# Kernel tuning notes

Measured on AMD Instinct MI355X. Metric: run time of the kernel, lower is better.

Reference implementation:

```python
import jax, jax.numpy as jnp
import numpy as np

D_MODEL = 1024
N_HEADS = 16
D_K = D_MODEL // N_HEADS


def setup_inputs() -> dict:
    key = jax.random.key(0)
    k1, k2, k3, k4, k5 = jax.random.split(key, 5)
    B, S = 2, 2048
    scale = 1.0 / np.sqrt(D_MODEL)
    return {
        "query": jax.random.normal(k1, (B, S, D_MODEL), dtype=jnp.float32),
        "mask": jnp.ones((B, S, S), dtype=jnp.int32),
        "W_qkv": jax.random.normal(k2, (D_MODEL, 3 * D_MODEL), dtype=jnp.float32) * scale,
        "b_qkv": jax.random.normal(k3, (3 * D_MODEL,), dtype=jnp.float32) * 0.02,
        "W_out": jax.random.normal(k4, (D_MODEL, D_MODEL), dtype=jnp.float32) * scale,
        "b_out": jax.random.normal(k5, (D_MODEL,), dtype=jnp.float32) * 0.02,
    }


def reference(query, mask, W_qkv, b_qkv, W_out, b_out):
    B, S, _ = query.shape
    # fused QKV projection (all from query, matching the torch module)
    qkv = query @ W_qkv + b_qkv                      # [B, S, 3*D]
    q, k, v = jnp.split(qkv, 3, axis=-1)
    # [B, H, S, d_k]
    q = q.reshape(B, S, N_HEADS, D_K).transpose(0, 2, 1, 3)
    k = k.reshape(B, S, N_HEADS, D_K).transpose(0, 2, 1, 3)
    v = v.reshape(B, S, N_HEADS, D_K).transpose(0, 2, 1, 3)
    # scaled dot-product attention with explicit scores
    scores = jnp.einsum("bhqd,bhkd->bhqk", q, k) / jnp.sqrt(jnp.float32(D_K))
    m = mask[:, None, :, :]                           # [B, 1, S, S] broadcast over heads
    scores = jnp.where(m == 0, jnp.float32(-1e9), scores)
    attn = jax.nn.softmax(scores, axis=-1)           # dropout p=0 in eval -> identity
    ctx = jnp.einsum("bhqk,bhkd->bhqd", attn, v)     # [B, H, S, d_k]
    ctx = ctx.transpose(0, 2, 1, 3).reshape(B, S, D_MODEL)
    return ctx @ W_out + b_out
```

## Files before the change

### kernel.cpp

```cpp
#include <hip/hip_runtime.h>
#include <stdint.h>
#include <stddef.h>

#define S_LEN 2048
#define NB    2
#define DM    1024
#define NH    16
#define DKH   64
#define NTOK  4096
#define QKV_N 3072
#define QSCALE 0.18033688f

typedef __attribute__((ext_vector_type(4))) float floatx4;
using half2v = __attribute__((ext_vector_type(2))) _Float16;
using half4v = __attribute__((ext_vector_type(4))) _Float16;
using half8v = __attribute__((ext_vector_type(8))) _Float16;
using fp16x2 = __attribute__((ext_vector_type(2))) __fp16;

#if __has_builtin(__builtin_amdgcn_exp2f)
#define EXP2F __builtin_amdgcn_exp2f
#else
#define EXP2F exp2f
#endif

__device__ __forceinline__ void glds16(const void* g, void* l) {
    __builtin_amdgcn_global_load_lds((const __attribute__((address_space(1))) void*)g,
                                     (__attribute__((address_space(3))) void*)l,
                                     16, 0, 0);
}

__global__ __launch_bounds__(256) void cast_f16_kernel(const float* __restrict__ in,
                                                       _Float16* __restrict__ out, int n4) {
    int i = blockIdx.x * blockDim.x + threadIdx.x;
    if (i < n4) {
        float4 v = ((const float4*)in)[i];
        half4v o = {(_Float16)v.x, (_Float16)v.y, (_Float16)v.z, (_Float16)v.w};
        ((half4v*)out)[i] = o;
    }
}

__global__ __launch_bounds__(1024) void transpose_cast_kernel(const float* __restrict__ in,
                                                              _Float16* __restrict__ out,
                                                              int R, int C) {
    __shared__ float t[32][33];
    int c0 = blockIdx.x * 32, r0 = blockIdx.y * 32;
    int x = threadIdx.x, y = threadIdx.y;
    t[y][x] = in[(size_t)(r0 + y) * C + c0 + x];
    __syncthreads();
    out[(size_t)(c0 + y) * R + r0 + x] = (_Float16)t[x][y];
}

__global__ __launch_bounds__(256) void mask_reduce_kernel(const int* __restrict__ mask,
                                                          int* __restrict__ f, int n4) {
    int i = blockIdx.x * blockDim.x + threadIdx.x;
    if (i < n4) {
        int4 v = ((const int4*)mask)[i];
        if (v.x == 0 || v.y == 0 || v.z == 0 || v.w == 0) *f = 0;
    }
}

__global__ __launch_bounds__(256) void transpose_v_kernel(const _Float16* __restrict__ qkv,
                                                          _Float16* __restrict__ vt) {
    __shared__ _Float16 t[64][68];
    int st = blockIdx.x * 64, h = blockIdx.y, b = blockIdx.z;
    int tid = threadIdx.x;
    #pragma unroll
    for (int p = 0; p < 4; ++p) {
        int idx = p * 1024 + tid * 4;
        int sl = idx >> 6, d0 = idx & 63;
        half4v v = *(const half4v*)(qkv + (size_t)(b * S_LEN + st + sl) * QKV_N + 2 * DM + h * DKH + d0);
        t[d0 + 0][sl] = v.x; t[d0 + 1][sl] = v.y; t[d0 + 2][sl] = v.z; t[d0 + 3][sl] = v.w;
    }
    __syncthreads();
    #pragma unroll
    for (int p = 0; p < 4; ++p) {
        int idx = p * 1024 + tid * 4;
        int d = idx >> 6, s0 = idx & 63;
        half4v v = {t[d][s0], t[d][s0 + 1], t[d][s0 + 2], t[d][s0 + 3]};
        *(half4v*)(vt + ((size_t)(b * NH + h) * DKH + d) * S_LEN + st + s0) = v;
    }
}

template <int FINAL, int BN>
__global__ __launch_bounds__(256) void gemm_bt_kernel(const _Float16* __restrict__ A,
                                                      const _Float16* __restrict__ Bt,
                                                      const float* __restrict__ bias,
                                                      float* __restrict__ Cf,
                                                      _Float16* __restrict__ Ch,
                                                      int M, int N, int K) {
    constexpr int NJ = BN / 32;
    __shared__ _Float16 As[128 * 64];
    __shared__ _Float16 Bs[BN * 64];

    const int nt = blockIdx.x, mt = blockIdx.y;
    const int tid = threadIdx.x, wave = tid >> 6, lane = tid & 63;
    const int quad = lane >> 4, l16 = lane & 15;
    const int wm = wave >> 1, wn = wave & 1;

    floatx4 acc[4][NJ];
    #pragma unroll
    for (int i = 0; i < 4; ++i)
        #pragma unroll
        for (int j = 0; j < NJ; ++j)
            #pragma unroll
            for (int r = 0; r < 4; ++r) acc[i][j][r] = 0.0f;

    const _Float16* Ab = A + (size_t)mt * 128 * K;
    const _Float16* Bb = Bt + (size_t)nt * BN * K;

    for (int kt = 0; kt < K; kt += 64) {
        #pragma unroll
        for (int p = 0; p < 4; ++p) {
            int slot = p * 256 + wave * 64 + lane;
            int row = slot >> 3, cc = slot & 7, c = cc ^ (row & 7);
            glds16(Ab + (size_t)row * K + kt + c * 8, As + (size_t)(p * 256 + wave * 64) * 8);
        }
        #pragma unroll
        for (int p = 0; p < BN / 32; ++p) {
            int slot = p * 256 + wave * 64 + lane;
            int row = slot >> 3, cc = slot & 7, c = cc ^ (row & 7);
            glds16(Bb + (size_t)row * K + kt + c * 8, Bs + (size_t)(p * 256 + wave * 64) * 8);
        }
        __syncthreads();

        #pragma unroll
        for (int kk = 0; kk < 2; ++kk) {
            half8v af[4], bfr[NJ];
            #pragma unroll
            for (int i = 0; i < 4; ++i) {
                int row = wm * 64 + i * 16 + l16;
                int c = (kk * 4 + quad) ^ (row & 7);
                af[i] = *(const half8v*)(As + row * 64 + c * 8);
            }
            #pragma unroll
            for (int j = 0; j < NJ; ++j) {
                int row = wn * (BN / 2) + j * 16 + l16;
                int c = (kk * 4 + quad) ^ (row & 7);
                bfr[j] = *(const half8v*)(Bs + row * 64 + c * 8);
            }
            #pragma unroll
            for (int i = 0; i < 4; ++i)
                #pragma unroll
                for (int j = 0; j < NJ; ++j)
                    acc[i][j] = __builtin_amdgcn_mfma_f32_16x16x32_f16(af[i], bfr[j], acc[i][j], 0, 0, 0);
        }
        __syncthreads();
    }

    #pragma unroll
    for (int j = 0; j < NJ; ++j) {
        int n = nt * BN + wn * (BN / 2) + j * 16 + l16;
        float bv = bias[n];
        float sc = (!FINAL && n < DM) ? QSCALE : 1.0f;
        #pragma unroll
        for (int i = 0; i < 4; ++i) {
            int m0 = mt * 128 + wm * 64 + i * 16 + quad * 4;
            #pragma unroll
            for (int r = 0; r < 4; ++r) {
                float v = (acc[i][j][r] + bv) * sc;
                if (FINAL) Cf[(size_t)(m0 + r) * N + n] = v;
                else       Ch[(size_t)(m0 + r) * QKV_N + n] = (_Float16)v;
            }
        }
    }
}

__global__ __launch_bounds__(256) void flash_kernel(const _Float16* __restrict__ qkv,
                                                    const _Float16* __restrict__ vt,
                                                    const int* __restrict__ mask,
                                                    const int* __restrict__ flag,
                                                    _Float16* __restrict__ Opart,
                                                    float* __restrict__ Lpart) {
    __shared__ _Float16 Ks[128 * 64];
    __shared__ _Float16 Vs[64 * 128];

    const int bh = blockIdx.x, qt = blockIdx.y, ks = blockIdx.z;
    const int b = bh >> 4, h = bh & 15;
    const int tid = threadIdx.x, wave = tid >> 6, lane = tid & 63;
    const int quad = lane >> 4, l16 = lane & 15;
    const int allones = (*flag != 0);

    const _Float16* qrow0 = qkv + (size_t)(b * S_LEN + qt * 128 + wave * 32 + l16) * QKV_N + h * DKH;
    const _Float16* qrow1 = qrow0 + (size_t)16 * QKV_N;
    half8v qa0 = *(const half8v*)(qrow0 + quad * 8);
    half8v qa1 = *(const half8v*)(qrow0 + 32 + quad * 8);
    half8v qb0 = *(const half8v*)(qrow1 + quad * 8);
    half8v qb1 = *(const half8v*)(qrow1 + 32 + quad * 8);

    const _Float16* kbase = qkv + (size_t)b * S_LEN * QKV_N + DM + h * DKH;
    const _Float16* vbase = vt + (size_t)(b * NH + h) * DKH * S_LEN;

    floatx4 oa[4], ob[4];
    #pragma unroll
    for (int c = 0; c < 4; ++c)
        #pragma unroll
        for (int r = 0; r < 4; ++r) { oa[c][r] = 0.0f; ob[c][r] = 0.0f; }
    float lsa = 0.0f, lsb = 0.0f;

    for (int kt = ks * 8; kt < ks * 8 + 8; ++kt) {
        #pragma unroll
        for (int p = 0; p < 4; ++p) {
            int slot = p * 256 + wave * 64 + lane;
            int row = slot >> 3, cc = slot & 7, c = cc ^ (row & 7);
            glds16(kbase + (size_t)(kt * 128 + row) * QKV_N + c * 8,
                   Ks + (size_t)(p * 256 + wave * 64) * 8);
        }
        #pragma unroll
        for (int p = 0; p < 4; ++p) {
            int slot = p * 256 + wave * 64 + lane;
            int row = slot >> 4, cc = slot & 15, c = cc ^ (row & 15);
            glds16(vbase + (size_t)row * S_LEN + kt * 128 + c * 8,
                   Vs + (size_t)(p * 256 + wave * 64) * 8);
        }
        __syncthreads();

        half4v pa[8], pb[8];
        #pragma unroll
        for (int j = 0; j < 8; ++j) {
            int rowk = j * 16 + l16;
            half8v a0 = *(const half8v*)(Ks + rowk * 64 + ((quad) ^ (rowk & 7)) * 8);
            half8v a1 = *(const half8v*)(Ks + rowk * 64 + ((4 + quad) ^ (rowk & 7)) * 8);
            floatx4 za, zb;
            #pragma unroll
            for (int r = 0; r < 4; ++r) { za[r] = 0.0f; zb[r] = 0.0f; }
            za = __builtin_amdgcn_mfma_f32_16x16x32_f16(a0, qa0, za, 0, 0, 0);
            za = __builtin_amdgcn_mfma_f32_16x16x32_f16(a1, qa1, za, 0, 0, 0);
            zb = __builtin_amdgcn_mfma_f32_16x16x32_f16(a0, qb0, zb, 0, 0, 0);
            zb = __builtin_amdgcn_mfma_f32_16x16x32_f16(a1, qb1, zb, 0, 0, 0);

            if (!allones) {
                for (int r = 0; r < 4; ++r) {
                    int s = kt * 128 + j * 16 + quad * 4 + r;
                    int qA = qt * 128 + wave * 32 + l16;
                    if (mask[((size_t)b * S_LEN + qA) * S_LEN + s] == 0) za[r] = -1e9f;
                    if (mask[((size_t)b * S_LEN + qA + 16) * S_LEN + s] == 0) zb[r] = -1e9f;
                }
            }

            float p0 = EXP2F(za[0]), p1 = EXP2F(za[1]), p2 = EXP2F(za[2]), p3 = EXP2F(za[3]);
            lsa += (p0 + p1) + (p2 + p3);
            fp16x2 lo = __builtin_amdgcn_cvt_pkrtz(p0, p1);
            fp16x2 hi = __builtin_amdgcn_cvt_pkrtz(p2, p3);
            half2v lo2 = __builtin_bit_cast(half2v, lo);
            half2v hi2 = __builtin_bit_cast(half2v, hi);
            half4v pka = {lo2.x, lo2.y, hi2.x, hi2.y};
            pa[j] = pka;

            p0 = EXP2F(zb[0]); p1 = EXP2F(zb[1]); p2 = EXP2F(zb[2]); p3 = EXP2F(zb[3]);
            lsb += (p0 + p1) + (p2 + p3);
            lo = __builtin_amdgcn_cvt_pkrtz(p0, p1);
            hi = __builtin_amdgcn_cvt_pkrtz(p2, p3);
            lo2 = __builtin_bit_cast(half2v, lo);
            hi2 = __builtin_bit_cast(half2v, hi);
            half4v pkb = {lo2.x, lo2.y, hi2.x, hi2.y};
            pb[j] = pkb;
        }

        #pragma unroll
        for (int j = 0; j < 8; ++j) {
            int g = 2 * j + (quad >> 1);
            #pragma unroll
            for (int c = 0; c < 4; ++c) {
                int rowv = c * 16 + l16;
                half4v bv = *(const half4v*)(Vs + rowv * 128 + ((g ^ (rowv & 15)) * 8) + (quad & 1) * 4);
                oa[c] = __builtin_amdgcn_mfma_f32_16x16x16f16(pa[j], bv, oa[c], 0, 0, 0);
                ob[c] = __builtin_amdgcn_mfma_f32_16x16x16f16(pb[j], bv, ob[c], 0, 0, 0);
            }
        }
        __syncthreads();
    }

    lsa += __shfl_xor(lsa, 16); lsa += __shfl_xor(lsa, 32);
    lsb += __shfl_xor(lsb, 16); lsb += __shfl_xor(lsb, 32);
    float lia[4], lib[4];
    #pragma unroll
    for (int r = 0; r < 4; ++r) {
        int src = (lane & 48) | ((lane >> 4) * 4 + r);
        float la_ = __shfl(lsa, src), lb_ = __shfl(lsb, src);
        lia[r] = la_ > 0.0f ? 1.0f / la_ : 0.0f;
        lib[r] = lb_ > 0.0f ? 1.0f / lb_ : 0.0f;
    }

    const size_t obase = ((size_t)(ks * 32 + bh) * 16 + qt) * (128 * 64);
    #pragma unroll
    for (int c = 0; c < 4; ++c)
        #pragma unroll
        for (int r = 0; r < 4; ++r) {
            int qq = wave * 32 + quad * 4 + r;
            Opart[obase + (size_t)qq * 64 + c * 16 + l16]        = (_Float16)(oa[c][r] * lia[r]);
            Opart[obase + (size_t)(qq + 16) * 64 + c * 16 + l16] = (_Float16)(ob[c][r] * lib[r]);
        }
    const int lbase = ((ks * 32 + bh) * 16 + qt) * 128;
    if (quad == 0) Lpart[lbase + wave * 32 + l16] = lsa;
    if (quad == 1) Lpart[lbase + wave * 32 + 16 + l16] = lsb;
}

__global__ __launch_bounds__(256) void combine_kernel(const _Float16* __restrict__ Opart,
                                                      const float* __restrict__ Lpart,
                                                      _Float16* __restrict__ ctx) {
    const int bh = blockIdx.x, qt = blockIdx.y;
    const int b = bh >> 4, h = bh & 15;
    const _Float16* Oa = Opart + ((size_t)(0 * 32 + bh) * 16 + qt) * (128 * 64);
    const _Float16* Ob = Opart + ((size_t)(1 * 32 + bh) * 16 + qt) * (128 * 64);
    const float* La = Lpart + ((0 * 32 + bh) * 16 + qt) * 128;
    const float* Lb = Lpart + ((1 * 32 + bh) * 16 + qt) * 128;
    #pragma unroll
    for (int k = 0; k < 4; ++k) {
        int i8 = k * 256 + threadIdx.x;
        int q = i8 >> 3, d0 = (i8 & 7) * 8;
        float la = La[q], lb = Lb[q];
        float s = la + lb;
        float w = s > 0.0f ? 1.0f / s : 0.0f;
        float wa = la * w, wb = lb * w;
        half8v va = *(const half8v*)(Oa + (size_t)i8 * 8);
        half8v vb = *(const half8v*)(Ob + (size_t)i8 * 8);
        half8v o;
        #pragma unroll
        for (int e = 0; e < 8; ++e)
            o[e] = (_Float16)((float)va[e] * wa + (float)vb[e] * wb);
        *(half8v*)(ctx + (size_t)(b * S_LEN + qt * 128 + q) * DM + h * DKH + d0) = o;
    }
}

extern "C" void kernel_launch(void* const* d_in, const int* in_sizes, int n_in,
                              void* d_out, int out_size, void* d_ws, size_t ws_size,
                              hipStream_t stream) {
    const float* query = (const float*)d_in[0];
    const int*   mask  = (const int*)d_in[1];
    const float* W_qkv = (const float*)d_in[2];
    const float* b_qkv = (const float*)d_in[3];
    const float* W_out = (const float*)d_in[4];
    const float* b_out = (const float*)d_in[5];
    float* out = (float*)d_out;

    char* w = (char*)d_ws;
    _Float16* qh    = (_Float16*)w;  w += (size_t)NTOK * DM * 2;
    _Float16* wqt   = (_Float16*)w;  w += (size_t)QKV_N * DM * 2;
    _Float16* wot   = (_Float16*)w;  w += (size_t)DM * DM * 2;
    _Float16* qkvh  = (_Float16*)w;  w += (size_t)NTOK * QKV_N * 2;
    _Float16* vt    = (_Float16*)w;  w += (size_t)NB * NH * DKH * S_LEN * 2;
    _Float16* Opart = (_Float16*)w;  w += (size_t)2 * NB * NH * 16 * 128 * 64 * 2;
    float*    Lpart = (float*)w;     w += (size_t)2 * NB * NH * 16 * 128 * 4;
    int*      flag  = (int*)w;
    _Float16* ctxh = qh;

    cast_f16_kernel<<<(NTOK * DM / 4 + 255) / 256, 256, 0, stream>>>(query, qh, NTOK * DM / 4);
    transpose_cast_kernel<<<dim3(QKV_N / 32, DM / 32), dim3(32, 32), 0, stream>>>(W_qkv, wqt, DM, QKV_N);
    transpose_cast_kernel<<<dim3(DM / 32, DM / 32), dim3(32, 32), 0, stream>>>(W_out, wot, DM, DM);
    hipMemsetAsync(flag, 1, 4, stream);
    mask_reduce_kernel<<<(NB * S_LEN * S_LEN / 4 + 255) / 256, 256, 0, stream>>>(
        mask, flag, NB * S_LEN * S_LEN / 4);

    gemm_bt_kernel<0, 128><<<dim3(QKV_N / 128, NTOK / 128), 256, 0, stream>>>(
        qh, wqt, b_qkv, nullptr, qkvh, NTOK, QKV_N, DM);

    transpose_v_kernel<<<dim3(S_LEN / 64, NH, NB), 256, 0, stream>>>(qkvh, vt);

    flash_kernel<<<dim3(NB * NH, S_LEN / 128, 2), 256, 0, stream>>>(
        qkvh, vt, mask, flag, Opart, Lpart);

    combine_kernel<<<dim3(NB * NH, S_LEN / 128), 256, 0, stream>>>(Opart, Lpart, ctxh);

    gemm_bt_kernel<1, 64><<<dim3(DM / 64, NTOK / 128), 256, 0, stream>>>(
        ctxh, wot, b_out, out, nullptr, NTOK, DM, DM);
}
```

Before: 231.9 us.

## Drop split-K attention and combine kernel, use 256-key tiles in flash

```diff
diff --git a/kernel.cpp b/kernel.cpp
--- a/kernel.cpp
+++ b/kernel.cpp
@@ -169,12 +169,11 @@
                                                     const _Float16* __restrict__ vt,
                                                     const int* __restrict__ mask,
                                                     const int* __restrict__ flag,
-                                                    _Float16* __restrict__ Opart,
-                                                    float* __restrict__ Lpart) {
-    __shared__ _Float16 Ks[128 * 64];
-    __shared__ _Float16 Vs[64 * 128];
-
-    const int bh = blockIdx.x, qt = blockIdx.y, ks = blockIdx.z;
+                                                    _Float16* __restrict__ ctx) {
+    __shared__ _Float16 Ks[256 * 64];
+    __shared__ _Float16 Vs[64 * 256];
+
+    const int bh = blockIdx.x, qt = blockIdx.y;
     const int b = bh >> 4, h = bh & 15;
     const int tid = threadIdx.x, wave = tid >> 6, lane = tid & 63;
     const int quad = lane >> 4, l16 = lane & 15;
@@ -197,74 +196,77 @@
         for (int r = 0; r < 4; ++r) { oa[c][r] = 0.0f; ob[c][r] = 0.0f; }
     float lsa = 0.0f, lsb = 0.0f;
 
-    for (int kt = ks * 8; kt < ks * 8 + 8; ++kt) {
-        #pragma unroll
-        for (int p = 0; p < 4; ++p) {
+    for (int kt = 0; kt < S_LEN / 256; ++kt) {
+        #pragma unroll
+        for (int p = 0; p < 8; ++p) {
             int slot = p * 256 + wave * 64 + lane;
             int row = slot >> 3, cc = slot & 7, c = cc ^ (row & 7);
-            glds16(kbase + (size_t)(kt * 128 + row) * QKV_N + c * 8,
+            glds16(kbase + (size_t)(kt * 256 + row) * QKV_N + c * 8,
                    Ks + (size_t)(p * 256 + wave * 64) * 8);
         }
         #pragma unroll
-        for (int p = 0; p < 4; ++p) {
+        for (int p = 0; p < 8; ++p) {
             int slot = p * 256 + wave * 64 + lane;
-            int row = slot >> 4, cc = slot & 15, c = cc ^ (row & 15);
-            glds16(vbase + (size_t)row * S_LEN + kt * 128 + c * 8,
+            int row = slot >> 5, cc = slot & 31, c = cc ^ (row & 15);
+            glds16(vbase + (size_t)row * S_LEN + kt * 256 + c * 8,
                    Vs + (size_t)(p * 256 + wave * 64) * 8);
         }
         __syncthreads();
 
-        half4v pa[8], pb[8];
-        #pragma unroll
-        for (int j = 0; j < 8; ++j) {
-            int rowk = j * 16 + l16;
-            half8v a0 = *(const half8v*)(Ks + rowk * 64 + ((quad) ^ (rowk & 7)) * 8);
-            half8v a1 = *(const half8v*)(Ks + rowk * 64 + ((4 + quad) ^ (rowk & 7)) * 8);
-            floatx4 za, zb;
-            #pragma unroll
-            for (int r = 0; r < 4; ++r) { za[r] = 0.0f; zb[r] = 0.0f; }
-            za = __builtin_amdgcn_mfma_f32_16x16x32_f16(a0, qa0, za, 0, 0, 0);
-            za = __builtin_amdgcn_mfma_f32_16x16x32_f16(a1, qa1, za, 0, 0, 0);
-            zb = __builtin_amdgcn_mfma_f32_16x16x32_f16(a0, qb0, zb, 0, 0, 0);
-            zb = __builtin_amdgcn_mfma_f32_16x16x32_f16(a1, qb1, zb, 0, 0, 0);
-
-            if (!allones) {
-                for (int r = 0; r < 4; ++r) {
-                    int s = kt * 128 + j * 16 + quad * 4 + r;
-                    int qA = qt * 128 + wave * 32 + l16;
-                    if (mask[((size_t)b * S_LEN + qA) * S_LEN + s] == 0) za[r] = -1e9f;
-                    if (mask[((size_t)b * S_LEN + qA + 16) * S_LEN + s] == 0) zb[r] = -1e9f;
+        #pragma unroll
+        for (int half = 0; half < 2; ++half) {
+            half4v pa[8], pb[8];
+            #pragma unroll
+            for (int j = 0; j < 8; ++j) {
+                int rowk = half * 128 + j * 16 + l16;
+                half8v a0 = *(const half8v*)(Ks + rowk * 64 + ((quad) ^ (rowk & 7)) * 8);
+                half8v a1 = *(const half8v*)(Ks + rowk * 64 + ((4 + quad) ^ (rowk & 7)) * 8);
+                floatx4 za, zb;
+                #pragma unroll
+                for (int r = 0; r < 4; ++r) { za[r] = 0.0f; zb[r] = 0.0f; }
+                za = __builtin_amdgcn_mfma_f32_16x16x32_f16(a0, qa0, za, 0, 0, 0);
+                za = __builtin_amdgcn_mfma_f32_16x16x32_f16(a1, qa1, za, 0, 0, 0);
+                zb = __builtin_amdgcn_mfma_f32_16x16x32_f16(a0, qb0, zb, 0, 0, 0);
+                zb = __builtin_amdgcn_mfma_f32_16x16x32_f16(a1, qb1, zb, 0, 0, 0);
+
+                if (!allones) {
+                    for (int r = 0; r < 4; ++r) {
+                        int s = kt * 256 + half * 128 + j * 16 + quad * 4 + r;
+                        int qA = qt * 128 + wave * 32 + l16;
+                        if (mask[((size_t)b * S_LEN + qA) * S_LEN + s] == 0) za[r] = -1e9f;
+                        if (mask[((size_t)b * S_LEN + qA + 16) * S_LEN + s] == 0) zb[r] = -1e9f;
+                    }
                 }
-            }
-
-            float p0 = EXP2F(za[0]), p1 = EXP2F(za[1]), p2 = EXP2F(za[2]), p3 = EXP2F(za[3]);
-            lsa += (p0 + p1) + (p2 + p3);
-            fp16x2 lo = __builtin_amdgcn_cvt_pkrtz(p0, p1);
-            fp16x2 hi = __builtin_amdgcn_cvt_pkrtz(p2, p3);
-            half2v lo2 = __builtin_bit_cast(half2v, lo);
-            half2v hi2 = __builtin_bit_cast(half2v, hi);
-            half4v pka = {lo2.x, lo2.y, hi2.x, hi2.y};
-            pa[j] = pka;
-
-            p0 = EXP2F(zb[0]); p1 = EXP2F(zb[1]); p2 = EXP2F(zb[2]); p3 = EXP2F(zb[3]);
-            lsb += (p0 + p1) + (p2 + p3);
-            lo = __builtin_amdgcn_cvt_pkrtz(p0, p1);
-            hi = __builtin_amdgcn_cvt_pkrtz(p2, p3);
-            lo2 = __builtin_bit_cast(half2v, lo);
-            hi2 = __builtin_bit_cast(half2v, hi);
-            half4v pkb = {lo2.x, lo2.y, hi2.x, hi2.y};
-            pb[j] = pkb;
-        }
-
-        #pragma unroll
-        for (int j = 0; j < 8; ++j) {
-            int g = 2 * j + (quad >> 1);
-            #pragma unroll
-            for (int c = 0; c < 4; ++c) {
-                int rowv = c * 16 + l16;
-                half4v bv = *(const half4v*)(Vs + rowv * 128 + ((g ^ (rowv & 15)) * 8) + (quad & 1) * 4);
-                oa[c] = __builtin_amdgcn_mfma_f32_16x16x16f16(pa[j], bv, oa[c], 0, 0, 0);
-                ob[c] = __builtin_amdgcn_mfma_f32_16x16x16f16(pb[j], bv, ob[c], 0, 0, 0);
+
+                float p0 = EXP2F(za[0]), p1 = EXP2F(za[1]), p2 = EXP2F(za[2]), p3 = EXP2F(za[3]);
+                lsa += (p0 + p1) + (p2 + p3);
+                fp16x2 lo = __builtin_amdgcn_cvt_pkrtz(p0, p1);
+                fp16x2 hi = __builtin_amdgcn_cvt_pkrtz(p2, p3);
+                half2v lo2 = __builtin_bit_cast(half2v, lo);
+                half2v hi2 = __builtin_bit_cast(half2v, hi);
+                half4v pka = {lo2.x, lo2.y, hi2.x, hi2.y};
+                pa[j] = pka;
+
+                p0 = EXP2F(zb[0]); p1 = EXP2F(zb[1]); p2 = EXP2F(zb[2]); p3 = EXP2F(zb[3]);
+                lsb += (p0 + p1) + (p2 + p3);
+                lo = __builtin_amdgcn_cvt_pkrtz(p0, p1);
+                hi = __builtin_amdgcn_cvt_pkrtz(p2, p3);
+                lo2 = __builtin_bit_cast(half2v, lo);
+                hi2 = __builtin_bit_cast(half2v, hi);
+                half4v pkb = {lo2.x, lo2.y, hi2.x, hi2.y};
+                pb[j] = pkb;
+            }
+
+            #pragma unroll
+            for (int j = 0; j < 8; ++j) {
+                int g = half * 16 + 2 * j + (quad >> 1);
+                #pragma unroll
+                for (int c = 0; c < 4; ++c) {
+                    int rowv = c * 16 + l16;
+                    half4v bv = *(const half4v*)(Vs + rowv * 256 + ((g ^ (rowv & 15)) * 8) + (quad & 1) * 4);
+                    oa[c] = __builtin_amdgcn_mfma_f32_16x16x16f16(pa[j], bv, oa[c], 0, 0, 0);
+                    ob[c] = __builtin_amdgcn_mfma_f32_16x16x16f16(pb[j], bv, ob[c], 0, 0, 0);
+                }
             }
         }
         __syncthreads();
@@ -276,50 +278,19 @@
     #pragma unroll
     for (int r = 0; r < 4; ++r) {
         int src = (lane & 48) | ((lane >> 4) * 4 + r);
-        float la_ = __shfl(lsa, src), lb_ = __shfl(lsb, src);
-        lia[r] = la_ > 0.0f ? 1.0f / la_ : 0.0f;
-        lib[r] = lb_ > 0.0f ? 1.0f / lb_ : 0.0f;
-    }
-
-    const size_t obase = ((size_t)(ks * 32 + bh) * 16 + qt) * (128 * 64);
+        lia[r] = 1.0f / __shfl(lsa, src);
+        lib[r] = 1.0f / __shfl(lsb, src);
+    }
+
     #pragma unroll
     for (int c = 0; c < 4; ++c)
         #pragma unroll
         for (int r = 0; r < 4; ++r) {
-            int qq = wave * 32 + quad * 4 + r;
-            Opart[obase + (size_t)qq * 64 + c * 16 + l16]        = (_Float16)(oa[c][r] * lia[r]);
-            Opart[obase + (size_t)(qq + 16) * 64 + c * 16 + l16] = (_Float16)(ob[c][r] * lib[r]);
-        }
-    const int lbase = ((ks * 32 + bh) * 16 + qt) * 128;
-    if (quad == 0) Lpart[lbase + wave * 32 + l16] = lsa;
-    if (quad == 1) Lpart[lbase + wave * 32 + 16 + l16] = lsb;
-}
-
-__global__ __launch_bounds__(256) void combine_kernel(const _Float16* __restrict__ Opart,
-                                                      const float* __restrict__ Lpart,
-                                                      _Float16* __restrict__ ctx) {
-    const int bh = blockIdx.x, qt = blockIdx.y;
-    const int b = bh >> 4, h = bh & 15;
-    const _Float16* Oa = Opart + ((size_t)(0 * 32 + bh) * 16 + qt) * (128 * 64);
-    const _Float16* Ob = Opart + ((size_t)(1 * 32 + bh) * 16 + qt) * (128 * 64);
-    const float* La = Lpart + ((0 * 32 + bh) * 16 + qt) * 128;
-    const float* Lb = Lpart + ((1 * 32 + bh) * 16 + qt) * 128;
-    #pragma unroll
-    for (int k = 0; k < 4; ++k) {
-        int i8 = k * 256 + threadIdx.x;
-        int q = i8 >> 3, d0 = (i8 & 7) * 8;
-        float la = La[q], lb = Lb[q];
-        float s = la + lb;
-        float w = s > 0.0f ? 1.0f / s : 0.0f;
-        float wa = la * w, wb = lb * w;
-        half8v va = *(const half8v*)(Oa + (size_t)i8 * 8);
-        half8v vb = *(const half8v*)(Ob + (size_t)i8 * 8);
-        half8v o;
-        #pragma unroll
-        for (int e = 0; e < 8; ++e)
-            o[e] = (_Float16)((float)va[e] * wa + (float)vb[e] * wb);
-        *(half8v*)(ctx + (size_t)(b * S_LEN + qt * 128 + q) * DM + h * DKH + d0) = o;
-    }
+            int qA = qt * 128 + wave * 32 + quad * 4 + r;
+            int col = h * DKH + c * 16 + l16;
+            ctx[(size_t)(b * S_LEN + qA) * DM + col]      = (_Float16)(oa[c][r] * lia[r]);
+            ctx[(size_t)(b * S_LEN + qA + 16) * DM + col] = (_Float16)(ob[c][r] * lib[r]);
+        }
 }
 
 extern "C" void kernel_launch(void* const* d_in, const int* in_sizes, int n_in,
@@ -339,8 +310,6 @@
     _Float16* wot   = (_Float16*)w;  w += (size_t)DM * DM * 2;
     _Float16* qkvh  = (_Float16*)w;  w += (size_t)NTOK * QKV_N * 2;
     _Float16* vt    = (_Float16*)w;  w += (size_t)NB * NH * DKH * S_LEN * 2;
-    _Float16* Opart = (_Float16*)w;  w += (size_t)2 * NB * NH * 16 * 128 * 64 * 2;
-    float*    Lpart = (float*)w;     w += (size_t)2 * NB * NH * 16 * 128 * 4;
     int*      flag  = (int*)w;
     _Float16* ctxh = qh;
 
@@ -356,10 +325,7 @@
 
     transpose_v_kernel<<<dim3(S_LEN / 64, NH, NB), 256, 0, stream>>>(qkvh, vt);
 
-    flash_kernel<<<dim3(NB * NH, S_LEN / 128, 2), 256, 0, stream>>>(
-        qkvh, vt, mask, flag, Opart, Lpart);
-
-    combine_kernel<<<dim3(NB * NH, S_LEN / 128), 256, 0, stream>>>(Opart, Lpart, ctxh);
+    flash_kernel<<<dim3(NB * NH, S_LEN / 128), 256, 0, stream>>>(qkvh, vt, mask, flag, ctxh);
 
     gemm_bt_kernel<1, 64><<<dim3(DM / 64, NTOK / 128), 256, 0, stream>>>(
         ctxh, wot, b_out, out, nullptr, NTOK, DM, DM);
```

Result: slower. 244.4 us (+5.4%).
